# Kernel optimization log

Hardware: AMD Instinct MI355X
Metric: run time of the kernel (lower is better)

## Reference

```python
import jax, jax.numpy as jnp
import numpy as np

T, HID = 2048, 4096
H = 32                 # num_heads
Q_LORA = 1536
KV_LORA = 512
D_NOPE = 128
D_ROPE = 64
D_QK = D_NOPE + D_ROPE  # 192
D_V = 128
EPS = 1e-6
THETA = 10000.0


def rmsnorm(x, scale):
    var = jnp.mean(x * x, axis=-1, keepdims=True)
    return x * jax.lax.rsqrt(var + EPS) * scale


def rope_interleaved(x, positions):
    # x: [T, h, D_ROPE], GPT-J interleaved style (rope_interleave=True -> not neox)
    half = D_ROPE // 2
    inv_freq = THETA ** (-jnp.arange(0, D_ROPE, 2, dtype=jnp.float32) / D_ROPE)  # [half]
    ang = positions.astype(jnp.float32)[:, None] * inv_freq[None, :]             # [T, half]
    cos = jnp.cos(ang)[:, None, :]
    sin = jnp.sin(ang)[:, None, :]
    x1 = x[..., 0::2]
    x2 = x[..., 1::2]
    o1 = x1 * cos - x2 * sin
    o2 = x1 * sin + x2 * cos
    return jnp.stack([o1, o2], axis=-1).reshape(x.shape)


def setup_inputs() -> dict:
    key = jax.random.key(0)
    ks = jax.random.split(key, 8)
    s = 0.02
    return {
        "hidden_states": jax.random.normal(ks[0], (T, HID), dtype=jnp.float32),
        "positions": jnp.arange(T, dtype=jnp.int32),
        "w_qa": jax.random.normal(ks[1], (HID, Q_LORA), dtype=jnp.float32) * s,
        "qa_ln_scale": jnp.ones((Q_LORA,), dtype=jnp.float32),
        "w_qb": jax.random.normal(ks[2], (Q_LORA, H * D_QK), dtype=jnp.float32) * s,
        "w_kva": jax.random.normal(ks[3], (HID, KV_LORA + D_ROPE), dtype=jnp.float32) * s,
        "kva_ln_scale": jnp.ones((KV_LORA,), dtype=jnp.float32),
        "w_uk": jax.random.normal(ks[4], (KV_LORA, H, D_NOPE), dtype=jnp.float32) * s,
        "w_uv": jax.random.normal(ks[5], (KV_LORA, H, D_V), dtype=jnp.float32) * s,
        "w_o": jax.random.normal(ks[6], (H * D_V, HID), dtype=jnp.float32) * s,
    }


def reference(hidden_states, positions, w_qa, qa_ln_scale, w_qb, w_kva,
              kva_ln_scale, w_uk, w_uv, w_o):
    # Q path: low-rank down-proj -> RMSNorm -> up-proj -> split nope/rope
    q_c = rmsnorm(hidden_states @ w_qa, qa_ln_scale)            # [T, Q_LORA]
    q = (q_c @ w_qb).reshape(T, H, D_QK)
    q_nope, q_rope = q[:, :, :D_NOPE], q[:, :, D_NOPE:]
    # KV path: joint down-proj -> split latent / rope key
    kv_a = hidden_states @ w_kva                                 # [T, KV_LORA + D_ROPE]
    compressed = rmsnorm(kv_a[:, :KV_LORA], kva_ln_scale)        # [T, KV_LORA]
    k_rope = kv_a[:, KV_LORA:][:, None, :]                       # [T, 1, D_ROPE]
    # partial RoPE on rope-dims only
    q_rope = rope_interleaved(q_rope, positions)
    k_rope = rope_interleaved(k_rope, positions)[:, 0, :]        # [T, D_ROPE]
    # Absorbed MQA: fold W_UK into Q, attend the shared latent
    ql_nope = jnp.einsum('thd,rhd->thr', q_nope, w_uk)           # [T, H, KV_LORA]
    scale = D_QK ** -0.5
    scores = (jnp.einsum('thr,sr->ths', ql_nope, compressed) +
              jnp.einsum('thd,sd->ths', q_rope, k_rope)) * scale # [T, H, T]
    causal = positions[:, None] >= positions[None, :]            # [T, T]
    scores = jnp.where(causal[:, None, :], scores, jnp.finfo(scores.dtype).min)
    probs = jax.nn.softmax(scores, axis=-1)
    o_latent = jnp.einsum('ths,sr->thr', probs, compressed)      # [T, H, KV_LORA]
    o_v = jnp.einsum('thr,rhd->thd', o_latent, w_uv)             # [T, H, D_V]
    out = o_v.reshape(T, H * D_V) @ w_o                          # [T, HID]
    return out
```

## Files before the change

kernel.cpp:

```cpp
#include <hip/hip_runtime.h>
#include <stdint.h>

typedef unsigned short u16;
typedef __attribute__((ext_vector_type(8))) short short8;
typedef __attribute__((ext_vector_type(4))) float floatx4;
typedef __attribute__((ext_vector_type(4))) unsigned short u16x4;

#define T_TOK 2048
#define NHEAD 32

__device__ __forceinline__ float bf2f(u16 u) { return __uint_as_float(((unsigned)u) << 16); }
__device__ __forceinline__ u16 f2bf(float f) {
    unsigned u = __float_as_uint(f);
    return (u16)((u + 0x7fffu + ((u >> 16) & 1u)) >> 16);
}

__device__ __forceinline__ floatx4 mfma16(short8 a, short8 b, floatx4 c) {
    return __builtin_amdgcn_mfma_f32_16x16x32_bf16(a, b, c, 0, 0, 0);
}

__global__ __launch_bounds__(256) void gemm_bt(
    const u16* __restrict__ A, const u16* __restrict__ B, void* __restrict__ Cp,
    int M, int N, int K, int lda, int ldb, int ldc,
    long sA, long sB, long sC, int c_bf16)
{
    __shared__ u16 As[128 * 32];
    __shared__ u16 Bs[128 * 32];
    const int z = blockIdx.z;
    A += (long)z * sA;
    B += (long)z * sB;
    const int tid  = threadIdx.x;
    const int wave = tid >> 6;
    const int lane = tid & 63;
    const long m0 = (long)blockIdx.y * 128;
    const long n0 = (long)blockIdx.x * 128;
    const int wm = (wave & 1) * 64;
    const int wn = (wave >> 1) * 64;
    const int lr = lane & 15;
    const int lk = (lane >> 4) * 8;

    const u16* Ag = A + (m0 + (tid >> 2)) * (long)lda + (tid & 3) * 8;
    const u16* Bg = B + (n0 + (tid >> 2)) * (long)ldb + (tid & 3) * 8;
    const long a64 = (long)64 * lda, b64 = (long)64 * ldb;

    floatx4 acc[4][4] = {};

    for (int k0 = 0; k0 < K; k0 += 32) {
        __syncthreads();
        __builtin_amdgcn_global_load_lds(
            (const __attribute__((address_space(1))) void*)(Ag + k0),
            (__attribute__((address_space(3))) void*)(As + wave * 512), 16, 0, 0);
        __builtin_amdgcn_global_load_lds(
            (const __attribute__((address_space(1))) void*)(Ag + k0 + a64),
            (__attribute__((address_space(3))) void*)(As + 2048 + wave * 512), 16, 0, 0);
        __builtin_amdgcn_global_load_lds(
            (const __attribute__((address_space(1))) void*)(Bg + k0),
            (__attribute__((address_space(3))) void*)(Bs + wave * 512), 16, 0, 0);
        __builtin_amdgcn_global_load_lds(
            (const __attribute__((address_space(1))) void*)(Bg + k0 + b64),
            (__attribute__((address_space(3))) void*)(Bs + 2048 + wave * 512), 16, 0, 0);
        __syncthreads();
        short8 af[4], bfr[4];
#pragma unroll
        for (int t = 0; t < 4; t++) {
            af[t]  = *(const short8*)&As[(wm + t * 16 + lr) * 32 + lk];
            bfr[t] = *(const short8*)&Bs[(wn + t * 16 + lr) * 32 + lk];
        }
#pragma unroll
        for (int mt = 0; mt < 4; mt++)
#pragma unroll
            for (int nt = 0; nt < 4; nt++)
                acc[mt][nt] = mfma16(af[mt], bfr[nt], acc[mt][nt]);
    }

    const int rbase = wm + (lane >> 4) * 4;
    if (c_bf16) {
        u16* C = (u16*)Cp + (long)z * sC;
#pragma unroll
        for (int mt = 0; mt < 4; mt++)
#pragma unroll
            for (int nt = 0; nt < 4; nt++)
#pragma unroll
                for (int r = 0; r < 4; r++) {
                    long row = m0 + rbase + mt * 16 + r;
                    long col = n0 + wn + nt * 16 + lr;
                    C[row * ldc + col] = f2bf(acc[mt][nt][r]);
                }
    } else {
        float* C = (float*)Cp + (long)z * sC;
#pragma unroll
        for (int mt = 0; mt < 4; mt++)
#pragma unroll
            for (int nt = 0; nt < 4; nt++)
#pragma unroll
                for (int r = 0; r < 4; r++) {
                    long row = m0 + rbase + mt * 16 + r;
                    long col = n0 + wn + nt * 16 + lr;
                    C[row * ldc + col] = acc[mt][nt][r];
                }
    }
}

#define ESCALE 0.10411754f

__global__ __launch_bounds__(256, 2) void flash_attn(
    const u16* __restrict__ Qp, const u16* __restrict__ Kp,
    const u16* __restrict__ Vp, u16* __restrict__ o_lat)
{
    __shared__ __align__(16) u16 Ks[18 * 1024];
    __shared__ __align__(16) u16 Vs[16 * 1024];
    __shared__ __align__(16) u16 Ps[64 * 40];
    __shared__ float ex[64];

    const int h = blockIdx.y;
    const int tid = threadIdx.x, wave = tid >> 6, lane = tid & 63;
    const int lr = lane & 15, hi = lane >> 4;
    const int wnp = wave * 128;

    const int st_idx = (wave << 9) + lane * 8;

    for (int half = 0; half < 2; half++) {
        const int qt = half ? (31 - (int)blockIdx.x) : (int)blockIdx.x;
        const int qb = qt * 64;
        const int nchunks = 2 * qt + 2;

        const u16* Qb = Qp + ((long)h * T_TOK + qb + wave * 16 + lr) * 576 + hi * 8;
        short8 qf[18];
#pragma unroll
        for (int s = 0; s < 18; s++)
            qf[s] = __builtin_nontemporal_load((const short8*)(Qb + s * 32));

        floatx4 oacc[4][8] = {};
        float l_part[4] = {};

        for (int c = 0; c < nchunks; c++) {
            const int jb = c * 32;
            const u16* ksrc = Kp + (long)c * 18432 + st_idx;
#pragma unroll
            for (int p = 0; p < 9; p++)
                __builtin_amdgcn_global_load_lds(
                    (const __attribute__((address_space(1))) void*)(ksrc + p * 2048),
                    (__attribute__((address_space(3))) void*)(Ks + st_idx + p * 2048), 16, 0, 0);
            const u16* vsrc = Vp + (long)c * 16384 + st_idx;
#pragma unroll
            for (int p = 0; p < 8; p++)
                __builtin_amdgcn_global_load_lds(
                    (const __attribute__((address_space(1))) void*)(vsrc + p * 2048),
                    (__attribute__((address_space(3))) void*)(Vs + st_idx + p * 2048), 16, 0, 0);
            __syncthreads();
            floatx4 sacc[2] = {};
#pragma unroll
            for (int s = 0; s < 18; s++) {
                short8 b0 = *(const short8*)(Ks + s * 1024 + lane * 8);
                short8 b1 = *(const short8*)(Ks + s * 1024 + 512 + lane * 8);
                sacc[0] = mfma16(qf[s], b0, sacc[0]);
                sacc[1] = mfma16(qf[s], b1, sacc[1]);
            }
            const int qg = qb + wave * 16 + hi * 4;
#pragma unroll
            for (int nt = 0; nt < 2; nt++) {
                const int kg = jb + nt * 16 + lr;
#pragma unroll
                for (int r = 0; r < 4; r++) {
                    float p = (kg <= qg + r) ? exp2f(sacc[nt][r] * ESCALE) : 0.0f;
                    l_part[r] += p;
                    Ps[(wave * 16 + hi * 4 + r) * 40 + nt * 16 + lr] = f2bf(p);
                }
            }
            __syncthreads();
            short8 pa[4];
#pragma unroll
            for (int mt = 0; mt < 4; mt++)
                pa[mt] = *(const short8*)(Ps + (mt * 16 + lr) * 40 + hi * 8);
#pragma unroll
            for (int nt = 0; nt < 8; nt++) {
                short8 vb = *(const short8*)(Vs + (wave * 8 + nt) * 512 + lane * 8);
#pragma unroll
                for (int mt = 0; mt < 4; mt++)
                    oacc[mt][nt] = mfma16(pa[mt], vb, oacc[mt][nt]);
            }
        }

#pragma unroll
        for (int r = 0; r < 4; r++) {
            float v = l_part[r];
            v += __shfl_xor(v, 1); v += __shfl_xor(v, 2);
            v += __shfl_xor(v, 4); v += __shfl_xor(v, 8);
            l_part[r] = v;
        }
        if (lr == 0) {
#pragma unroll
            for (int r = 0; r < 4; r++) ex[wave * 16 + hi * 4 + r] = l_part[r];
        }
        __syncthreads();
        const long obase = (long)h * T_TOK + qb;
#pragma unroll
        for (int mt = 0; mt < 4; mt++)
#pragma unroll
            for (int r = 0; r < 4; r++) {
                const int row = mt * 16 + hi * 4 + r;
                const float inv = 1.0f / ex[row];
#pragma unroll
                for (int nt = 0; nt < 8; nt++)
                    __builtin_nontemporal_store(
                        f2bf(oacc[mt][nt][r] * inv),
                        o_lat + (obase + row) * 512 + wnp + nt * 16 + lr);
            }
        __syncthreads();
    }
}

__global__ __launch_bounds__(256) void cast_bf16_k(const float* __restrict__ src,
                                                   u16* __restrict__ dst, long n)
{
    long i = ((long)blockIdx.x * 256 + threadIdx.x) * 4;
    if (i + 3 < n) {
        float4 v = *(const float4*)(src + i);
        u16x4 o = { f2bf(v.x), f2bf(v.y), f2bf(v.z), f2bf(v.w) };
        *(u16x4*)(dst + i) = o;
    }
}

__global__ void transpose_cast(const float* __restrict__ src, u16* __restrict__ dst,
                               int R, int C, int Cpad)
{
    __shared__ float tile[32][33];
    const int cb = blockIdx.x * 32, rb = blockIdx.y * 32;
    for (int i = threadIdx.y; i < 32; i += 8) {
        int r = rb + i, c = cb + threadIdx.x;
        tile[i][threadIdx.x] = (r < R && c < C) ? src[(long)r * C + c] : 0.0f;
    }
    __syncthreads();
    for (int i = threadIdx.y; i < 32; i += 8) {
        int c = cb + i, r = rb + threadIdx.x;
        if (c < Cpad && r < R) dst[(long)c * R + r] = f2bf(tile[threadIdx.x][i]);
    }
}

__global__ __launch_bounds__(256) void permute_wuv(const float* __restrict__ src,
                                                   u16* __restrict__ dst)
{
    int idx = blockIdx.x * 256 + threadIdx.x;
    int r = idx & 511;
    int hd = idx >> 9;
    int d = hd & 127, h = hd >> 7;
    dst[idx] = f2bf(src[(long)r * 4096 + h * 128 + d]);
}

__global__ __launch_bounds__(256) void rmsnorm_rows(const u16* __restrict__ in,
                                                    const float* __restrict__ gamma,
                                                    u16* __restrict__ out, int n, float invn)
{
    const long base = (long)blockIdx.x * n;
    const int tid = threadIdx.x, wave = tid >> 6, lane = tid & 63;
    __shared__ float red[4];
    float ss = 0.f;
    for (int i = tid; i < n; i += 256) { float x = bf2f(in[base + i]); ss += x * x; }
    for (int o = 32; o > 0; o >>= 1) ss += __shfl_xor(ss, o);
    if (lane == 0) red[wave] = ss;
    __syncthreads();
    ss = red[0] + red[1] + red[2] + red[3];
    const float r = rsqrtf(ss * invn + 1e-6f);
    for (int i = tid; i < n; i += 256) {
        float x = bf2f(in[base + i]);
        out[base + i] = f2bf(x * r * gamma[i]);
    }
}

__global__ __launch_bounds__(256) void kv_post(const u16* __restrict__ kva,
                                               const float* __restrict__ gamma,
                                               const int* __restrict__ pos,
                                               u16* __restrict__ Kp2, u16* __restrict__ Vp2)
{
    const int t = blockIdx.x;
    const long base = (long)t * 640;
    const int tid = threadIdx.x, wave = tid >> 6, lane = tid & 63;
    __shared__ float red[4];
    float ss = 0.f;
    for (int i = tid; i < 512; i += 256) { float x = bf2f(kva[base + i]); ss += x * x; }
    for (int o = 32; o > 0; o >>= 1) ss += __shfl_xor(ss, o);
    if (lane == 0) red[wave] = ss;
    __syncthreads();
    ss = red[0] + red[1] + red[2] + red[3];
    const float r = rsqrtf(ss * (1.0f / 512.0f) + 1e-6f);
    const int rr = t & 31, j = t >> 5;
    {
        const long vbase = (long)j * 16384;
        const int e = rr & 7, lhi = (rr >> 3) * 16;
        for (int i = tid; i < 512; i += 256) {
            float x = bf2f(kva[base + i]) * r * gamma[i];
            const int ct = i >> 4, l = lhi + (i & 15);
            Vp2[vbase + ct * 512 + l * 8 + e] = f2bf(x);
        }
    }
    if (tid < 72) {
        const int g  = tid;
        const int i0 = g * 8;
        const int s  = i0 >> 5, p = s >> 1, sb = s & 1, hi2 = (i0 & 31) >> 3;
        const int wv = sb * 2 + (rr >> 4);
        const int ln = (rr & 15) + 16 * hi2;
        const long gidx = (long)j * 18432 + p * 2048 + wv * 512 + ln * 8;
        short8 outv;
        if (g < 64) {
#pragma unroll
            for (int m = 0; m < 8; m++) {
                float x = bf2f(kva[base + i0 + m]) * r * gamma[i0 + m];
                ((u16*)&outv)[m] = f2bf(x);
            }
        } else {
#pragma unroll
            for (int q = 0; q < 4; q++) {
                int jj = ((i0 - 512) >> 1) + q;
                float invf = powf(10000.0f, -(float)jj / 32.0f);
                float ang = (float)pos[t] * invf;
                float sn, cs;
                sincosf(ang, &sn, &cs);
                float x1 = bf2f(kva[base + 512 + 2 * jj]);
                float x2 = bf2f(kva[base + 512 + 2 * jj + 1]);
                ((u16*)&outv)[2 * q]     = f2bf(x1 * cs - x2 * sn);
                ((u16*)&outv)[2 * q + 1] = f2bf(x1 * sn + x2 * cs);
            }
        }
        *(short8*)(Kp2 + gidx) = outv;
    }
}

__global__ __launch_bounds__(256) void rope_q(const u16* __restrict__ q,
                                              const int* __restrict__ pos,
                                              u16* __restrict__ Qp)
{
    int idx = blockIdx.x * 256 + threadIdx.x;
    int j = idx & 31;
    int h = (idx >> 5) & 31;
    int t = idx >> 10;
    float invf = powf(10000.0f, -(float)j / 32.0f);
    float ang = (float)pos[t] * invf;
    float sn, cs;
    sincosf(ang, &sn, &cs);
    long qb = (long)t * 6144 + h * 192 + 128 + 2 * j;
    float x1 = bf2f(q[qb]), x2 = bf2f(q[qb + 1]);
    long ob = (long)h * T_TOK * 576 + (long)t * 576 + 512 + 2 * j;
    Qp[ob]     = f2bf(x1 * cs - x2 * sn);
    Qp[ob + 1] = f2bf(x1 * sn + x2 * cs);
}

extern "C" void kernel_launch(void* const* d_in, const int* in_sizes, int n_in,
                              void* d_out, int out_size, void* d_ws, size_t ws_size,
                              hipStream_t stream)
{
    const float* hidden = (const float*)d_in[0];
    const int* positions = (const int*)d_in[1];
    const float* w_qa  = (const float*)d_in[2];
    const float* qa_g  = (const float*)d_in[3];
    const float* w_qb  = (const float*)d_in[4];
    const float* w_kva = (const float*)d_in[5];
    const float* kva_g = (const float*)d_in[6];
    const float* w_uk  = (const float*)d_in[7];
    const float* w_uv  = (const float*)d_in[8];
    const float* w_o   = (const float*)d_in[9];

    char* ws = (char*)d_ws;
    u16* o_lat   = (u16*)(ws + 0);
    u16* qc      = (u16*)(ws + 0);
    u16* q       = (u16*)(ws + 6291456);
    u16* hid_bf  = (u16*)(ws + 31457280);
    u16* wqa_t   = (u16*)(ws + 48234496);
    u16* qc_raw  = (u16*)(ws + 60817408);
    u16* wqb_t   = (u16*)(ws + 67108864);
    u16* wkva_t  = (u16*)(ws + 85983232);
    u16* wuk_b   = (u16*)(ws + 91226112);
    u16* wuv_t   = (u16*)(ws + 95420416);
    u16* wo_t    = (u16*)(ws + 99614720);
    u16* kva_raw = (u16*)(ws + 133169152);
    u16* Kp      = (u16*)(ws + 135790592);
    u16* Vp      = (u16*)(ws + 138149888);
    u16* Qp      = (u16*)(ws + 140247040);
    u16* o_v     = Qp;

    cast_bf16_k<<<8192, 256, 0, stream>>>(hidden, hid_bf, 8388608);
    transpose_cast<<<dim3(48, 128),  dim3(32, 8), 0, stream>>>(w_qa,  wqa_t,  4096, 1536, 1536);
    transpose_cast<<<dim3(192, 48),  dim3(32, 8), 0, stream>>>(w_qb,  wqb_t,  1536, 6144, 6144);
    transpose_cast<<<dim3(20, 128),  dim3(32, 8), 0, stream>>>(w_kva, wkva_t, 4096, 576,  640);
    cast_bf16_k<<<2048, 256, 0, stream>>>(w_uk, wuk_b, 2097152);
    permute_wuv<<<8192, 256, 0, stream>>>(w_uv, wuv_t);
    transpose_cast<<<dim3(128, 128), dim3(32, 8), 0, stream>>>(w_o,   wo_t,   4096, 4096, 4096);

    gemm_bt<<<dim3(12, 16, 1), 256, 0, stream>>>(hid_bf, wqa_t, qc_raw,
        2048, 1536, 4096, 4096, 4096, 1536, 0, 0, 0, 1);
    gemm_bt<<<dim3(5, 16, 1), 256, 0, stream>>>(hid_bf, wkva_t, kva_raw,
        2048, 640, 4096, 4096, 4096, 640, 0, 0, 0, 1);
    rmsnorm_rows<<<2048, 256, 0, stream>>>(qc_raw, qa_g, qc, 1536, 1.0f / 1536.0f);
    kv_post<<<2048, 256, 0, stream>>>(kva_raw, kva_g, positions, Kp, Vp);

    gemm_bt<<<dim3(48, 16, 1), 256, 0, stream>>>(qc, wqb_t, q,
        2048, 6144, 1536, 1536, 1536, 6144, 0, 0, 0, 1);
    rope_q<<<8192, 256, 0, stream>>>(q, positions, Qp);
    gemm_bt<<<dim3(4, 16, 32), 256, 0, stream>>>(q, wuk_b, Qp,
        2048, 512, 128, 6144, 4096, 576, 192, 128, (long)2048 * 576, 1);

    flash_attn<<<dim3(16, 32), 256, 0, stream>>>(Qp, Kp, Vp, o_lat);

    gemm_bt<<<dim3(1, 16, 32), 256, 0, stream>>>(o_lat, wuv_t, o_v,
        2048, 128, 512, 512, 512, 4096, (long)2048 * 512, 65536, 128, 1);
    gemm_bt<<<dim3(32, 16, 1), 256, 0, stream>>>(o_v, wo_t, d_out,
        2048, 4096, 4096, 4096, 4096, 4096, 0, 0, 0, 0);
}
```

Baseline: 848.7 us.

## Prefetch next K/V chunk into LDS during current chunk's compute in flash attention

Moves the global-to-LDS staging of K and V out of the top of each chunk iteration. K for the next chunk is issued after the score phase and V for the next chunk after the PV phase, with the first chunk staged before the loop and re-staged between halves. This lets the asynchronous load latency overlap with MFMA work instead of stalling at the chunk barrier. It adds manual lgkmcnt waits and barriers, and the correctness of reusing single LDS buffers depends on the waitcnt/vmcnt handling of async LDS loads.

```diff
diff --git a/kernel.cpp b/kernel.cpp
--- a/kernel.cpp
+++ b/kernel.cpp
@@ -103,6 +103,25 @@
 
 #define ESCALE 0.10411754f
 
+#define STAGE_K(CIDX)                                                          \
+    {                                                                          \
+        const u16* ksrc_ = Kp + (long)(CIDX) * 18432 + st_idx;                 \
+        _Pragma("unroll")                                                      \
+        for (int p_ = 0; p_ < 9; p_++)                                         \
+            __builtin_amdgcn_global_load_lds(                                  \
+                (const __attribute__((address_space(1))) void*)(ksrc_ + p_ * 2048), \
+                (__attribute__((address_space(3))) void*)(Ks + st_idx + p_ * 2048), 16, 0, 0); \
+    }
+#define STAGE_V(CIDX)                                                          \
+    {                                                                          \
+        const u16* vsrc_ = Vp + (long)(CIDX) * 16384 + st_idx;                 \
+        _Pragma("unroll")                                                      \
+        for (int p_ = 0; p_ < 8; p_++)                                         \
+            __builtin_amdgcn_global_load_lds(                                  \
+                (const __attribute__((address_space(1))) void*)(vsrc_ + p_ * 2048), \
+                (__attribute__((address_space(3))) void*)(Vs + st_idx + p_ * 2048), 16, 0, 0); \
+    }
+
 __global__ __launch_bounds__(256, 2) void flash_attn(
     const u16* __restrict__ Qp, const u16* __restrict__ Kp,
     const u16* __restrict__ Vp, u16* __restrict__ o_lat)
@@ -119,6 +138,9 @@
 
     const int st_idx = (wave << 9) + lane * 8;
 
+    STAGE_K(0);
+    STAGE_V(0);
+
     for (int half = 0; half < 2; half++) {
         const int qt = half ? (31 - (int)blockIdx.x) : (int)blockIdx.x;
         const int qb = qt * 64;
@@ -135,18 +157,6 @@
 
         for (int c = 0; c < nchunks; c++) {
             const int jb = c * 32;
-            const u16* ksrc = Kp + (long)c * 18432 + st_idx;
-#pragma unroll
-            for (int p = 0; p < 9; p++)
-                __builtin_amdgcn_global_load_lds(
-                    (const __attribute__((address_space(1))) void*)(ksrc + p * 2048),
-                    (__attribute__((address_space(3))) void*)(Ks + st_idx + p * 2048), 16, 0, 0);
-            const u16* vsrc = Vp + (long)c * 16384 + st_idx;
-#pragma unroll
-            for (int p = 0; p < 8; p++)
-                __builtin_amdgcn_global_load_lds(
-                    (const __attribute__((address_space(1))) void*)(vsrc + p * 2048),
-                    (__attribute__((address_space(3))) void*)(Vs + st_idx + p * 2048), 16, 0, 0);
             __syncthreads();
             floatx4 sacc[2] = {};
 #pragma unroll
@@ -168,6 +178,7 @@
                 }
             }
             __syncthreads();
+            if (c + 1 < nchunks) STAGE_K(c + 1);
             short8 pa[4];
 #pragma unroll
             for (int mt = 0; mt < 4; mt++)
@@ -178,6 +189,15 @@
 #pragma unroll
                 for (int mt = 0; mt < 4; mt++)
                     oacc[mt][nt] = mfma16(pa[mt], vb, oacc[mt][nt]);
+            }
+            asm volatile("s_waitcnt lgkmcnt(0)" ::: "memory");
+            __builtin_amdgcn_s_barrier();
+            __builtin_amdgcn_sched_barrier(0);
+            if (c + 1 < nchunks) {
+                STAGE_V(c + 1);
+            } else if (half == 0) {
+                STAGE_K(0);
+                STAGE_V(0);
             }
         }
 
@@ -192,7 +212,9 @@
 #pragma unroll
             for (int r = 0; r < 4; r++) ex[wave * 16 + hi * 4 + r] = l_part[r];
         }
-        __syncthreads();
+        asm volatile("s_waitcnt lgkmcnt(0)" ::: "memory");
+        __builtin_amdgcn_s_barrier();
+        __builtin_amdgcn_sched_barrier(0);
         const long obase = (long)h * T_TOK + qb;
 #pragma unroll
         for (int mt = 0; mt < 4; mt++)
@@ -206,7 +228,6 @@
                         f2bf(oacc[mt][nt][r] * inv),
                         o_lat + (obase + row) * 512 + wnp + nt * 16 + lr);
             }
-        __syncthreads();
     }
 }
 
```

After: 890.2 us. 1.05x slower.
